# Kernel optimization log

Hardware: AMD Instinct MI355X
Metric: run time of the kernel (lower is better)

## Reference

```python
import jax, jax.numpy as jnp
import numpy as np

DIM = 1024
H = 16
HD = DIM // H
SCALE = HD ** -0.5


def _split_heads(t):
    B, N, C = t.shape
    return t.reshape(B, N, H, C // H).transpose(0, 2, 1, 3)  # [B,H,N,hd]


def _attn(q, k, v):
    # q,k,v: [B,H,N,hd]
    scores = jnp.einsum('bhqd,bhkd->bhqk', q, k) * SCALE
    a = jax.nn.softmax(scores, axis=-1)
    o = jnp.einsum('bhqk,bhkd->bhqd', a, v)
    B, Hh, N, d = o.shape
    return o.transpose(0, 2, 1, 3).reshape(B, N, Hh * d)


def setup_inputs() -> dict:
    key = jax.random.key(0)
    ks = jax.random.split(key, 18)
    B, N = 4, 2048
    s = DIM ** -0.5
    inp = {
        'f_a': jax.random.normal(ks[0], (B, N, DIM), jnp.float32),
        'f_b': jax.random.normal(ks[1], (B, N, DIM), jnp.float32),
    }
    names = ['q_a', 'k_a', 'v_a', 'q_b', 'k_b', 'v_b', 'proj']
    for i, nm in enumerate(names):
        inp[f'W_{nm}'] = jax.random.normal(ks[2 + 2 * i], (DIM, DIM), jnp.float32) * s
        inp[f'b_{nm}'] = jnp.zeros((DIM,), jnp.float32)
    inp['ln_gamma'] = jnp.ones((DIM,), jnp.float32)
    inp['ln_beta'] = jnp.zeros((DIM,), jnp.float32)
    return inp


def _layernorm(x, gamma, beta, eps=1e-5):
    mu = jnp.mean(x, axis=-1, keepdims=True)
    var = jnp.mean((x - mu) ** 2, axis=-1, keepdims=True)
    return (x - mu) * jax.lax.rsqrt(var + eps) * gamma + beta


def reference(f_a, f_b,
              W_q_a, b_q_a, W_k_a, b_k_a, W_v_a, b_v_a,
              W_q_b, b_q_b, W_k_b, b_k_b, W_v_b, b_v_b,
              W_proj, b_proj, ln_gamma, ln_beta):
    lin = lambda x, W, b: x @ W.T + b  # torch Linear convention
    f_ta = _attn(_split_heads(lin(f_a, W_q_a, b_q_a)),
                 _split_heads(lin(f_b, W_k_b, b_k_b)),
                 _split_heads(lin(f_b, W_v_b, b_v_b)))
    f_tb = _attn(_split_heads(lin(f_b, W_q_b, b_q_b)),
                 _split_heads(lin(f_a, W_k_a, b_k_a)),
                 _split_heads(lin(f_a, W_v_a, b_v_a)))
    fused = _layernorm(f_ta + f_tb, ln_gamma, ln_beta)
    return lin(fused, W_proj, b_proj)
```

## Files before the change

kernel.cpp:

```cpp
#include <hip/hip_runtime.h>
#include <hip/hip_bf16.h>
#include <stdint.h>

typedef __bf16 bf16_t;
typedef __attribute__((ext_vector_type(8))) __bf16 bf16x8;
typedef __attribute__((ext_vector_type(4))) __bf16 bf16x4;
typedef __attribute__((ext_vector_type(4))) float f32x4;

#define LOG2E 1.4426950408889634f
#define EXP2 __builtin_amdgcn_exp2f
#define MFIX 12.0f

struct Ptr7 { const float* p[7]; };
struct Bias6 { const float* p[6]; };

__device__ __forceinline__ void gload16(const void* g, void* l) {
  __builtin_amdgcn_global_load_lds(
      (const __attribute__((address_space(1))) unsigned int*)g,
      (__attribute__((address_space(3))) unsigned int*)l,
      16, 0, 0);
}

__global__ __launch_bounds__(256)
void cvt_act(const float* __restrict__ a, const float* __restrict__ b,
             bf16_t* __restrict__ d) {
  const float* s = blockIdx.y ? b : a;
  int i = (blockIdx.x * 256 + threadIdx.x) * 4;
  f32x4 v = *(const f32x4*)(s + i);
  bf16x4 o;
  o[0] = (bf16_t)v[0]; o[1] = (bf16_t)v[1];
  o[2] = (bf16_t)v[2]; o[3] = (bf16_t)v[3];
  *(bf16x4*)(d + (size_t)blockIdx.y * 8388608 + i) = o;
}

__global__ __launch_bounds__(256)
void cvt_w(Ptr7 s, bf16_t* __restrict__ d) {
  int z = blockIdx.y;
  int i = (blockIdx.x * 256 + threadIdx.x) * 4;
  f32x4 v = *(const f32x4*)(s.p[z] + i);
  bf16x4 o;
  o[0] = (bf16_t)v[0]; o[1] = (bf16_t)v[1];
  o[2] = (bf16_t)v[2]; o[3] = (bf16_t)v[3];
  *(bf16x4*)(d + (size_t)z * 1048576 + i) = o;
}

template <typename OutT>
__device__ __forceinline__
void gemm_core(const bf16_t* __restrict__ A, const bf16_t* __restrict__ W,
               const float* __restrict__ bias, OutT* __restrict__ C,
               int M, int N, int K, float alpha, int vt,
               bf16_t* sm) {
  bf16_t* As = sm;
  bf16_t* Ws = sm + 8192;

  const int tid = threadIdx.x;
  const int lane = tid & 63;
  const int wid = tid >> 6;
  const int wr = wid >> 1, wc = wid & 1;
  const int g = lane >> 4, r15 = lane & 15;

  const int m0 = blockIdx.y * 128;
  const int n0 = blockIdx.x * 128;

  const int srow = tid >> 2;
  const int sslot = (tid & 3) ^ (srow & 3);
  const bf16_t* aS = A + (int64_t)(m0 + srow) * K + sslot * 8;
  const bf16_t* wS = W + (int64_t)(n0 + srow) * K + sslot * 8;

#define STAGE_G(buf, koff) do {                                          \
    gload16(aS + (koff),          &As[(buf) * 4096 + wid * 512]);        \
    gload16(aS + (koff) + 64 * K, &As[(buf) * 4096 + 2048 + wid * 512]); \
    gload16(wS + (koff),          &Ws[(buf) * 4096 + wid * 512]);        \
    gload16(wS + (koff) + 64 * K, &Ws[(buf) * 4096 + 2048 + wid * 512]); \
  } while (0)

  f32x4 acc[4][4] = {};
  STAGE_G(0, 0);
  __syncthreads();

  const int KT = K >> 5;
  int cur = 0;
  for (int kt = 0; kt < KT; ++kt) {
    if (kt + 1 < KT) STAGE_G(cur ^ 1, (kt + 1) * 32);
    bf16x8 af[4], wf[4];
#pragma unroll
    for (int i = 0; i < 4; ++i) {
      const int ar = wr * 64 + i * 16 + r15;
      af[i] = *(const bf16x8*)&As[cur * 4096 + ar * 32 + (((g ^ (ar & 3))) << 3)];
      const int br = wc * 64 + i * 16 + r15;
      wf[i] = *(const bf16x8*)&Ws[cur * 4096 + br * 32 + (((g ^ (br & 3))) << 3)];
    }
    __builtin_amdgcn_s_setprio(1);
#pragma unroll
    for (int i = 0; i < 4; ++i)
#pragma unroll
      for (int j = 0; j < 4; ++j)
        acc[i][j] = __builtin_amdgcn_mfma_f32_16x16x32_bf16(af[i], wf[j], acc[i][j], 0, 0, 0);
    __builtin_amdgcn_s_setprio(0);
    __syncthreads();
    cur ^= 1;
  }
#undef STAGE_G

  if (vt) {
    bf16_t* T = sm;
#pragma unroll
    for (int j = 0; j < 4; ++j) {
      const int colL = wc * 64 + j * 16 + r15;
      const float bv = bias[n0 + colL];
#pragma unroll
      for (int i = 0; i < 4; ++i) {
        const int rowL = wr * 64 + i * 16 + g * 4;
        bf16x4 o4;
#pragma unroll
        for (int q = 0; q < 4; ++q) o4[q] = (bf16_t)((acc[i][j][q] + bv) * alpha);
        *(bf16x4*)&T[colL * 136 + rowL] = o4;
      }
    }
    __syncthreads();
    const int bidx = m0 >> 11;
    const int nb = m0 & 2047;
    OutT* base = C + (int64_t)(bidx * 1024 + n0) * 2048 + nb;
    const int lane16 = tid & 15, c16 = tid >> 4;
#pragma unroll
    for (int p = 0; p < 8; ++p) {
      const int colL = p * 16 + c16;
      bf16x8 v = *(const bf16x8*)&T[colL * 136 + lane16 * 8];
      *(bf16x8*)(base + (int64_t)colL * 2048 + lane16 * 8) = v;
    }
  } else {
#pragma unroll
    for (int j = 0; j < 4; ++j) {
      const int col = n0 + wc * 64 + j * 16 + r15;
      const float bv = bias[col];
#pragma unroll
      for (int i = 0; i < 4; ++i) {
        const int row = m0 + wr * 64 + i * 16 + g * 4;
#pragma unroll
        for (int q = 0; q < 4; ++q) {
          float v = (acc[i][j][q] + bv) * alpha;
          C[(int64_t)(row + q) * N + col] = (OutT)v;
        }
      }
    }
  }
}

__global__ __launch_bounds__(256)
void qkv_gemm(const bf16_t* __restrict__ fa, const bf16_t* __restrict__ fb,
              const bf16_t* __restrict__ Wall, Bias6 bs,
              bf16_t* __restrict__ outb, float aQ) {
  __shared__ __align__(16) bf16_t sm[17408];
  const int z = blockIdx.z;
  const bf16_t* A = (z < 3) ? fa : fb;
  const bf16_t* W = Wall + (size_t)z * 1048576;
  const float alpha = (z == 0 || z == 3) ? aQ : 1.f;
  const int vt = (z == 2 || z == 5) ? 1 : 0;
  bf16_t* C = outb + (size_t)z * 8388608;
  gemm_core<bf16_t>(A, W, bs.p[z], C, 8192, 1024, 1024, alpha, vt, sm);
}

__global__ __launch_bounds__(256)
void gemm_proj(const bf16_t* __restrict__ A, const bf16_t* __restrict__ W,
               const float* __restrict__ bias, float* __restrict__ C) {
  __shared__ __align__(16) bf16_t sm[16384];
  gemm_core<float>(A, W, bias, C, 8192, 1024, 1024, 1.f, 0, sm);
}

__global__ __launch_bounds__(256, 3)
void attn_fused(const bf16_t* __restrict__ Q0, const bf16_t* __restrict__ K0,
                const bf16_t* __restrict__ VT0, bf16_t* __restrict__ O0,
                const bf16_t* __restrict__ Q1, const bf16_t* __restrict__ K1,
                const bf16_t* __restrict__ VT1, bf16_t* __restrict__ O1) {
  __shared__ __align__(16) bf16_t Ks[2][64 * 64];
  __shared__ __align__(16) bf16_t Vs[2][64 * 64];
  __shared__ __align__(16) bf16_t Ps[4][32 * 64];

  const int tid = threadIdx.x, lane = tid & 63, wid = tid >> 6;
  const int g = lane >> 4, r15 = lane & 15;
  const int bh = blockIdx.y, b = bh >> 4, h = bh & 15;
  const int zz = blockIdx.z;
  const bf16_t* Q = zz ? Q1 : Q0;
  const bf16_t* Kg = zz ? K1 : K0;
  const bf16_t* VT = zz ? VT1 : VT0;
  bf16_t* O = zz ? O1 : O0;

  const int q0 = blockIdx.x * 128 + wid * 32;
  const int sw4 = (r15 & 7) << 4;

  const bf16_t* qp = Q + (int64_t)(b * 2048 + q0 + r15) * 1024 + h * 64 + g * 8;
  bf16x8 qf[2][2];
  qf[0][0] = *(const bf16x8*)(qp);
  qf[0][1] = *(const bf16x8*)(qp + 32);
  qf[1][0] = *(const bf16x8*)(qp + 16 * 1024);
  qf[1][1] = *(const bf16x8*)(qp + 16 * 1024 + 32);

  const int srow = tid >> 3;
  const int sslot = (tid & 7) ^ (srow & 7);
  const bf16_t* kP = Kg + (int64_t)(b * 2048 + srow) * 1024 + h * 64 + sslot * 8;
  const bf16_t* vP = VT + (int64_t)(bh * 64 + srow) * 2048 + sslot * 8;

#define STAGE_KV(BUF) do {                                       \
    gload16(kP,             &Ks[BUF][wid * 512]);                \
    gload16(kP + 32 * 1024, &Ks[BUF][2048 + wid * 512]);         \
    gload16(vP,             &Vs[BUF][wid * 512]);                \
    gload16(vP + 32 * 2048, &Vs[BUF][2048 + wid * 512]);         \
  } while (0)

  f32x4 ot[2][4] = {};
  float l[2] = {0.f, 0.f};
  char* const pb0 = (char*)&Ps[wid][0];

  STAGE_KV(0);
  __syncthreads();

#define TILE(BUF, ISLAST) do {                                                \
    if (!(ISLAST)) { kP += 64 * 1024; vP += 64; STAGE_KV(BUF ^ 1); }          \
    bf16x8 ka[4], kc[4];                                                      \
    _Pragma("unroll")                                                         \
    for (int kb = 0; kb < 4; ++kb) {                                          \
      const int krow = kb * 16 + r15;                                         \
      const int rsw = (krow & 7) << 4;                                        \
      const char* kbase = (const char*)&Ks[BUF][0] + krow * 128;              \
      ka[kb] = *(const bf16x8*)(kbase + ((g * 16) ^ rsw));                    \
      kc[kb] = *(const bf16x8*)(kbase + ((64 + g * 16) ^ rsw));               \
    }                                                                         \
    f32x4 st[2][4];                                                           \
    __builtin_amdgcn_s_setprio(1);                                            \
    _Pragma("unroll")                                                         \
    for (int u = 0; u < 2; ++u)                                               \
      _Pragma("unroll")                                                       \
      for (int kb = 0; kb < 4; ++kb) {                                        \
        f32x4 zv = {0.f, 0.f, 0.f, 0.f};                                      \
        zv = __builtin_amdgcn_mfma_f32_16x16x32_bf16(ka[kb], qf[u][0], zv, 0, 0, 0); \
        st[u][kb] = __builtin_amdgcn_mfma_f32_16x16x32_bf16(kc[kb], qf[u][1], zv, 0, 0, 0); \
      }                                                                       \
    __builtin_amdgcn_s_setprio(0);                                            \
    _Pragma("unroll")                                                         \
    for (int u = 0; u < 2; ++u) {                                             \
      char* pbase = pb0 + (u * 16 + r15) * 128;                               \
      _Pragma("unroll")                                                       \
      for (int kb = 0; kb < 4; ++kb) {                                        \
        bf16x4 pv;                                                            \
        _Pragma("unroll")                                                     \
        for (int j = 0; j < 4; ++j) {                                         \
          float p = EXP2(st[u][kb][j] - MFIX); l[u] += p; pv[j] = (bf16_t)p;  \
        }                                                                     \
        *(bf16x4*)(pbase + ((kb * 32 + g * 8) ^ sw4)) = pv;                   \
      }                                                                       \
    }                                                                         \
    bf16x8 va[4], vc[4];                                                      \
    _Pragma("unroll")                                                         \
    for (int db = 0; db < 4; ++db) {                                          \
      const int drow = db * 16 + r15;                                         \
      const int rsw = (drow & 7) << 4;                                        \
      const char* vbase = (const char*)&Vs[BUF][0] + drow * 128;              \
      va[db] = *(const bf16x8*)(vbase + ((g * 16) ^ rsw));                    \
      vc[db] = *(const bf16x8*)(vbase + ((64 + g * 16) ^ rsw));               \
    }                                                                         \
    bf16x8 pA[2], pB[2];                                                      \
    _Pragma("unroll")                                                         \
    for (int u = 0; u < 2; ++u) {                                             \
      const char* pbase = pb0 + (u * 16 + r15) * 128;                         \
      pA[u] = *(const bf16x8*)(pbase + ((g * 16) ^ sw4));                     \
      pB[u] = *(const bf16x8*)(pbase + ((64 + g * 16) ^ sw4));                \
    }                                                                         \
    __builtin_amdgcn_s_setprio(1);                                            \
    _Pragma("unroll")                                                         \
    for (int u = 0; u < 2; ++u)                                               \
      _Pragma("unroll")                                                       \
      for (int db = 0; db < 4; ++db) {                                        \
        ot[u][db] = __builtin_amdgcn_mfma_f32_16x16x32_bf16(va[db], pA[u], ot[u][db], 0, 0, 0); \
        ot[u][db] = __builtin_amdgcn_mfma_f32_16x16x32_bf16(vc[db], pB[u], ot[u][db], 0, 0, 0); \
      }                                                                       \
    __builtin_amdgcn_s_setprio(0);                                            \
    __syncthreads();                                                          \
  } while (0)

  for (int it = 0; it < 16; ++it) {
    TILE(0, false);
    TILE(1, it == 15);
  }
#undef TILE
#undef STAGE_KV

#pragma unroll
  for (int u = 0; u < 2; ++u) {
    float lu = l[u];
    lu += __shfl_xor(lu, 16);
    lu += __shfl_xor(lu, 32);
    const float inv = 1.f / lu;
    bf16_t* op = O + (int64_t)(b * 2048 + q0 + u * 16 + r15) * 1024 + h * 64;
#pragma unroll
    for (int db = 0; db < 4; ++db) {
      bf16x4 o4;
#pragma unroll
      for (int j = 0; j < 4; ++j) o4[j] = (bf16_t)(ot[u][db][j] * inv);
      *(bf16x4*)(op + db * 16 + g * 4) = o4;
    }
  }
}

__global__ __launch_bounds__(256)
void ln_fuse(const bf16_t* __restrict__ A, const bf16_t* __restrict__ B,
             const float* __restrict__ gamma, const float* __restrict__ beta,
             bf16_t* __restrict__ out) {
  const int row = blockIdx.x, tid = threadIdx.x;
  const bf16x4 xa = *(const bf16x4*)(A + (int64_t)row * 1024 + tid * 4);
  const bf16x4 xb = *(const bf16x4*)(B + (int64_t)row * 1024 + tid * 4);
  f32x4 x;
#pragma unroll
  for (int j = 0; j < 4; ++j) x[j] = (float)xa[j] + (float)xb[j];
  float s = x[0] + x[1] + x[2] + x[3];
  float q = x[0] * x[0] + x[1] * x[1] + x[2] * x[2] + x[3] * x[3];
#pragma unroll
  for (int o = 32; o; o >>= 1) { s += __shfl_down(s, o); q += __shfl_down(q, o); }
  __shared__ float ss[4], qq[4];
  if ((tid & 63) == 0) { ss[tid >> 6] = s; qq[tid >> 6] = q; }
  __syncthreads();
  s = ss[0] + ss[1] + ss[2] + ss[3];
  q = qq[0] + qq[1] + qq[2] + qq[3];
  const float mu = s * (1.f / 1024.f);
  const float var = q * (1.f / 1024.f) - mu * mu;
  const float rcp = rsqrtf(var + 1e-5f);
  const int c = tid * 4;
  const f32x4 g4 = *(const f32x4*)(gamma + c);
  const f32x4 b4 = *(const f32x4*)(beta + c);
  bf16x4 o;
#pragma unroll
  for (int j = 0; j < 4; ++j) o[j] = (bf16_t)((x[j] - mu) * rcp * g4[j] + b4[j]);
  *(bf16x4*)(out + (int64_t)row * 1024 + c) = o;
}

extern "C" void kernel_launch(void* const* d_in, const int* in_sizes, int n_in,
                              void* d_out, int out_size, void* d_ws, size_t ws_size,
                              hipStream_t stream) {
  const float* f_a = (const float*)d_in[0];
  const float* f_b = (const float*)d_in[1];
  const float* W[7];
  const float* bv[7];
  for (int i = 0; i < 7; ++i) {
    W[i] = (const float*)d_in[2 + 2 * i];
    bv[i] = (const float*)d_in[3 + 2 * i];
  }
  const float* ln_g = (const float*)d_in[16];
  const float* ln_b = (const float*)d_in[17];
  float* out = (float*)d_out;

  char* ws = (char*)d_ws;
  const size_t MB = 1ull << 20;
  bf16_t* fa_bf = (bf16_t*)(ws + 0 * MB);
  bf16_t* fb_bf = fa_bf + 8388608;
  bf16_t* Wbf   = (bf16_t*)(ws + 32 * MB);
  bf16_t* qkv   = (bf16_t*)(ws + 48 * MB);
  bf16_t* Qa  = (bf16_t*)(ws + 48 * MB);
  bf16_t* Ka  = (bf16_t*)(ws + 64 * MB);
  bf16_t* VaT = (bf16_t*)(ws + 80 * MB);
  bf16_t* Qb  = (bf16_t*)(ws + 96 * MB);
  bf16_t* Kb  = (bf16_t*)(ws + 112 * MB);
  bf16_t* VbT = (bf16_t*)(ws + 128 * MB);
  bf16_t* f_ta = fa_bf;
  bf16_t* f_tb = fb_bf;
  bf16_t* fused = Qa;

  const float aQ = 0.125f * LOG2E;

  cvt_act<<<dim3(8192, 2), 256, 0, stream>>>(f_a, f_b, fa_bf);
  Ptr7 p7; for (int i = 0; i < 7; ++i) p7.p[i] = W[i];
  cvt_w<<<dim3(1024, 7), 256, 0, stream>>>(p7, Wbf);

  Bias6 b6; for (int i = 0; i < 6; ++i) b6.p[i] = bv[i];
  qkv_gemm<<<dim3(8, 64, 6), 256, 0, stream>>>(fa_bf, fb_bf, Wbf, b6, qkv, aQ);

  attn_fused<<<dim3(16, 64, 2), 256, 0, stream>>>(Qa, Kb, VbT, f_ta,
                                                  Qb, Ka, VaT, f_tb);

  ln_fuse<<<8192, 256, 0, stream>>>(f_ta, f_tb, ln_g, ln_b, fused);

  gemm_proj<<<dim3(8, 64), 256, 0, stream>>>(fused, Wbf + 6 * 1048576, bv[6], out);
}
```

Baseline: 402.9 us.

## Remap block IDs for XCD locality and halve attention P scratch

```diff
diff --git a/kernel.cpp b/kernel.cpp
--- a/kernel.cpp
+++ b/kernel.cpp
@@ -48,7 +48,7 @@
 __device__ __forceinline__
 void gemm_core(const bf16_t* __restrict__ A, const bf16_t* __restrict__ W,
                const float* __restrict__ bias, OutT* __restrict__ C,
-               int M, int N, int K, float alpha, int vt,
+               int m0, int n0, int N, int K, float alpha, int vt,
                bf16_t* sm) {
   bf16_t* As = sm;
   bf16_t* Ws = sm + 8192;
@@ -58,9 +58,6 @@
   const int wid = tid >> 6;
   const int wr = wid >> 1, wc = wid & 1;
   const int g = lane >> 4, r15 = lane & 15;
-
-  const int m0 = blockIdx.y * 128;
-  const int n0 = blockIdx.x * 128;
 
   const int srow = tid >> 2;
   const int sslot = (tid & 3) ^ (srow & 3);
@@ -151,41 +148,56 @@
               const bf16_t* __restrict__ Wall, Bias6 bs,
               bf16_t* __restrict__ outb, float aQ) {
   __shared__ __align__(16) bf16_t sm[17408];
-  const int z = blockIdx.z;
+  const int lin = blockIdx.x + 8 * (blockIdx.y + 64 * blockIdx.z);
+  const int pos = (lin & 7) * 384 + (lin >> 3);
+  const int z = pos >> 9;
+  const int rem = pos & 511;
+  const int m0 = (rem >> 3) * 128;
+  const int n0 = (rem & 7) * 128;
   const bf16_t* A = (z < 3) ? fa : fb;
   const bf16_t* W = Wall + (size_t)z * 1048576;
   const float alpha = (z == 0 || z == 3) ? aQ : 1.f;
   const int vt = (z == 2 || z == 5) ? 1 : 0;
   bf16_t* C = outb + (size_t)z * 8388608;
-  gemm_core<bf16_t>(A, W, bs.p[z], C, 8192, 1024, 1024, alpha, vt, sm);
+  gemm_core<bf16_t>(A, W, bs.p[z], C, m0, n0, 1024, 1024, alpha, vt, sm);
 }
 
 __global__ __launch_bounds__(256)
 void gemm_proj(const bf16_t* __restrict__ A, const bf16_t* __restrict__ W,
                const float* __restrict__ bias, float* __restrict__ C) {
   __shared__ __align__(16) bf16_t sm[16384];
-  gemm_core<float>(A, W, bias, C, 8192, 1024, 1024, 1.f, 0, sm);
-}
-
-__global__ __launch_bounds__(256, 3)
+  const int lin = blockIdx.x + 8 * blockIdx.y;
+  const int pos = (lin & 7) * 64 + (lin >> 3);
+  const int m0 = (pos >> 3) * 128;
+  const int n0 = (pos & 7) * 128;
+  gemm_core<float>(A, W, bias, C, m0, n0, 1024, 1024, 1.f, 0, sm);
+}
+
+__global__ __launch_bounds__(256, 4)
 void attn_fused(const bf16_t* __restrict__ Q0, const bf16_t* __restrict__ K0,
                 const bf16_t* __restrict__ VT0, bf16_t* __restrict__ O0,
                 const bf16_t* __restrict__ Q1, const bf16_t* __restrict__ K1,
                 const bf16_t* __restrict__ VT1, bf16_t* __restrict__ O1) {
   __shared__ __align__(16) bf16_t Ks[2][64 * 64];
   __shared__ __align__(16) bf16_t Vs[2][64 * 64];
-  __shared__ __align__(16) bf16_t Ps[4][32 * 64];
+  __shared__ __align__(16) bf16_t Ps[4][16 * 64];
 
   const int tid = threadIdx.x, lane = tid & 63, wid = tid >> 6;
   const int g = lane >> 4, r15 = lane & 15;
-  const int bh = blockIdx.y, b = bh >> 4, h = bh & 15;
-  const int zz = blockIdx.z;
+
+  const int lin = blockIdx.x + 16 * (blockIdx.y + 64 * blockIdx.z);
+  const int pos = (lin & 7) * 256 + (lin >> 3);
+  const int qblk = pos & 15;
+  const int bh = (pos >> 4) & 63;
+  const int zz = pos >> 10;
+  const int b = bh >> 4, h = bh & 15;
+
   const bf16_t* Q = zz ? Q1 : Q0;
   const bf16_t* Kg = zz ? K1 : K0;
   const bf16_t* VT = zz ? VT1 : VT0;
   bf16_t* O = zz ? O1 : O0;
 
-  const int q0 = blockIdx.x * 128 + wid * 32;
+  const int q0 = qblk * 128 + wid * 32;
   const int sw4 = (r15 & 7) << 4;
 
   const bf16_t* qp = Q + (int64_t)(b * 2048 + q0 + r15) * 1024 + h * 64 + g * 8;
@@ -210,6 +222,7 @@
   f32x4 ot[2][4] = {};
   float l[2] = {0.f, 0.f};
   char* const pb0 = (char*)&Ps[wid][0];
+  char* const pbase = pb0 + r15 * 128;
 
   STAGE_KV(0);
   __syncthreads();
@@ -236,9 +249,17 @@
         st[u][kb] = __builtin_amdgcn_mfma_f32_16x16x32_bf16(kc[kb], qf[u][1], zv, 0, 0, 0); \
       }                                                                       \
     __builtin_amdgcn_s_setprio(0);                                            \
+    bf16x8 va[4], vc[4];                                                      \
+    _Pragma("unroll")                                                         \
+    for (int db = 0; db < 4; ++db) {                                          \
+      const int drow = db * 16 + r15;                                         \
+      const int rsw = (drow & 7) << 4;                                        \
+      const char* vbase = (const char*)&Vs[BUF][0] + drow * 128;              \
+      va[db] = *(const bf16x8*)(vbase + ((g * 16) ^ rsw));                    \
+      vc[db] = *(const bf16x8*)(vbase + ((64 + g * 16) ^ rsw));               \
+    }                                                                         \
     _Pragma("unroll")                                                         \
     for (int u = 0; u < 2; ++u) {                                             \
-      char* pbase = pb0 + (u * 16 + r15) * 128;                               \
       _Pragma("unroll")                                                       \
       for (int kb = 0; kb < 4; ++kb) {                                        \
         bf16x4 pv;                                                            \
@@ -248,32 +269,16 @@
         }                                                                     \
         *(bf16x4*)(pbase + ((kb * 32 + g * 8) ^ sw4)) = pv;                   \
       }                                                                       \
-    }                                                                         \
-    bf16x8 va[4], vc[4];                                                      \
-    _Pragma("unroll")                                                         \
-    for (int db = 0; db < 4; ++db) {                                          \
-      const int drow = db * 16 + r15;                                         \
-      const int rsw = (drow & 7) << 4;                                        \
-      const char* vbase = (const char*)&Vs[BUF][0] + drow * 128;              \
-      va[db] = *(const bf16x8*)(vbase + ((g * 16) ^ rsw));                    \
-      vc[db] = *(const bf16x8*)(vbase + ((64 + g * 16) ^ rsw));               \
-    }                                                                         \
-    bf16x8 pA[2], pB[2];                                                      \
-    _Pragma("unroll")                                                         \
-    for (int u = 0; u < 2; ++u) {                                             \
-      const char* pbase = pb0 + (u * 16 + r15) * 128;                         \
-      pA[u] = *(const bf16x8*)(pbase + ((g * 16) ^ sw4));                     \
-      pB[u] = *(const bf16x8*)(pbase + ((64 + g * 16) ^ sw4));                \
-    }                                                                         \
-    __builtin_amdgcn_s_setprio(1);                                            \
-    _Pragma("unroll")                                                         \
-    for (int u = 0; u < 2; ++u)                                               \
+      bf16x8 pA = *(const bf16x8*)(pbase + ((g * 16) ^ sw4));                 \
+      bf16x8 pB = *(const bf16x8*)(pbase + ((64 + g * 16) ^ sw4));            \
+      __builtin_amdgcn_s_setprio(1);                                          \
       _Pragma("unroll")                                                       \
       for (int db = 0; db < 4; ++db) {                                        \
-        ot[u][db] = __builtin_amdgcn_mfma_f32_16x16x32_bf16(va[db], pA[u], ot[u][db], 0, 0, 0); \
-        ot[u][db] = __builtin_amdgcn_mfma_f32_16x16x32_bf16(vc[db], pB[u], ot[u][db], 0, 0, 0); \
+        ot[u][db] = __builtin_amdgcn_mfma_f32_16x16x32_bf16(va[db], pA, ot[u][db], 0, 0, 0); \
+        ot[u][db] = __builtin_amdgcn_mfma_f32_16x16x32_bf16(vc[db], pB, ot[u][db], 0, 0, 0); \
       }                                                                       \
-    __builtin_amdgcn_s_setprio(0);                                            \
+      __builtin_amdgcn_s_setprio(0);                                          \
+    }                                                                         \
     __syncthreads();                                                          \
   } while (0)
 
```

Result: slower. 610.8 us (+51.6%).
